# Optimization experiments

Measured on AMD Instinct MI355X. Metric: run time of the kernel, lower is better.

The kernel has to match this reference:

```python
import jax, jax.numpy as jnp
import numpy as np

N_HEAD = 16
THETA = 10000.0


def _freqs_cos_sin(head_dim, seq_len):
    # matches precompute_freqs_cis: freqs = 1/theta^(arange(0,dim,2)/dim), outer with t
    inv = 1.0 / (THETA ** (jnp.arange(0, head_dim, 2, dtype=jnp.float32) / head_dim))
    t = jnp.arange(seq_len, dtype=jnp.float32)
    ang = jnp.outer(t, inv)  # [L, head_dim//2]
    return jnp.cos(ang), jnp.sin(ang)


def _rope(x, cos, sin):
    # x: [B, H, L, D]; pairs are interleaved (view_as_complex on (..., D//2, 2))
    x1 = x[..., 0::2]
    x2 = x[..., 1::2]
    out_re = x1 * cos - x2 * sin
    out_im = x1 * sin + x2 * cos
    return jnp.stack([out_re, out_im], axis=-1).reshape(x.shape)


def setup_inputs() -> dict:
    key = jax.random.key(0)
    ks = jax.random.split(key, 11)
    B, L, D = 2, 2048, 1024
    s = 0.02
    return {
        "q": jax.random.normal(ks[0], (B, L, D), jnp.float32),
        "k": jax.random.normal(ks[1], (B, L, D), jnp.float32),
        "v": jax.random.normal(ks[2], (B, L, D), jnp.float32),
        "wq": jax.random.normal(ks[3], (D, D), jnp.float32) * s,
        "bq": jax.random.normal(ks[4], (D,), jnp.float32) * s,
        "wk": jax.random.normal(ks[5], (D, D), jnp.float32) * s,
        "bk": jax.random.normal(ks[6], (D,), jnp.float32) * s,
        "wv": jax.random.normal(ks[7], (D, D), jnp.float32) * s,
        "bv": jax.random.normal(ks[8], (D,), jnp.float32) * s,
        "wo": jax.random.normal(ks[9], (D, D), jnp.float32) * s,
        "bo": jax.random.normal(ks[10], (D,), jnp.float32) * s,
    }


def reference(q, k, v, wq, bq, wk, bk, wv, bv, wo, bo):
    B, L, D = q.shape
    Hd = D // N_HEAD
    # projections (nn.Linear: x @ W^T + b)
    qp = q @ wq.T + bq
    kp = k @ wk.T + bk
    vp = v @ wv.T + bv
    # split: [B, L, D] -> [B, H, L, Hd]
    def split(t):
        return t.reshape(B, L, N_HEAD, Hd).transpose(0, 2, 1, 3)
    qh, kh, vh = split(qp), split(kp), split(vp)
    cos, sin = _freqs_cos_sin(Hd, L)  # [L, Hd//2], broadcasts over B, H
    qh = _rope(qh, cos, sin)
    kh = _rope(kh, cos, sin)
    # scaled dot-product attention (no mask)
    scores = jnp.einsum("bhqd,bhkd->bhqk", qh, kh) / jnp.sqrt(jnp.float32(Hd))
    attn = jax.nn.softmax(scores, axis=-1)
    out = jnp.einsum("bhqk,bhkd->bhqd", attn, vh)
    # concat heads and output projection
    out = out.transpose(0, 2, 1, 3).reshape(B, L, D)
    return out @ wo.T + bo
```

## Files before the change

kernel.cpp:

```cpp
#include <hip/hip_runtime.h>
#include <hip/hip_bf16.h>
#include <math.h>

#define BB 2
#define LL 2048
#define DD 1024
#define NH 16
#define HD 64

typedef short v8s __attribute__((ext_vector_type(8)));
typedef float v4f __attribute__((ext_vector_type(4)));
typedef float v16f __attribute__((ext_vector_type(16)));

__device__ __forceinline__ float b2f(unsigned short b) {
  union { unsigned int u; float f; } c; c.u = ((unsigned int)b) << 16; return c.f;
}
__device__ __forceinline__ unsigned short f2b(float x) {
  union { float f; unsigned int u; } c; c.f = x;
  unsigned int u = c.u;
  u += 0x7fffu + ((u >> 16) & 1u);
  return (unsigned short)(u >> 16);
}
__device__ __forceinline__ unsigned int asu(float x) {
  union { float f; unsigned int u; } c; c.f = x; return c.u;
}
__device__ __forceinline__ unsigned int pk2(float lo, float hi) {
  return __builtin_amdgcn_perm(asu(hi), asu(lo), 0x07060302u);
}

__device__ __forceinline__ void gload16(const void* g, void* l) {
  __builtin_amdgcn_global_load_lds(
      (const __attribute__((address_space(1))) void*)g,
      (__attribute__((address_space(3))) void*)l, 16, 0, 0);
}

struct CastArgs { const float* s[7]; unsigned short* d[7]; };
__global__ void cast_all(CastArgs a) {
  int z = blockIdx.z;
  int t = (z < 12) ? (z >> 2) : (z - 9);
  int off = (z < 12) ? ((z & 3) << 18) : 0;
  int i = off + blockIdx.x * blockDim.x + threadIdx.x;
  float4 v = ((const float4*)a.s[t])[i];
  ushort4 o;
  o.x = f2b(v.x); o.y = f2b(v.y); o.z = f2b(v.z); o.w = f2b(v.w);
  ((ushort4*)a.d[t])[i] = o;
}

__global__ void freqs_kernel(float* __restrict__ ctab, float* __restrict__ stab) {
  int id = blockIdx.x * blockDim.x + threadIdx.x;
  int t = id >> 5, i = id & 31;
  float inv = powf(10000.0f, -(float)(2 * i) / 64.0f);
  float ang = (float)t * inv;
  ctab[id] = cosf(ang);
  stab[id] = sinf(ang);
}

template <typename OutT>
__device__ __forceinline__ void gemm_body(const unsigned short* __restrict__ X,
                                          const unsigned short* __restrict__ W,
                                          const float* __restrict__ bias,
                                          OutT* __restrict__ Y,
                                          int M, int N, int K) {
  __shared__ __align__(16) unsigned short As[128 * 64];
  __shared__ __align__(16) unsigned short Bs[128 * 64];
  const int tid = threadIdx.x;
  const int lane = tid & 63, wave = tid >> 6;
  const int quad = lane >> 4, l16 = lane & 15;
  const int bn0 = blockIdx.x * 128;
  const int bm0 = blockIdx.y * 128;
  const int wm = (wave >> 1) * 64, wn = (wave & 1) * 64;

  const v4f vzero = {0.f, 0.f, 0.f, 0.f};
  v4f acc[4][4];
#pragma unroll
  for (int i = 0; i < 4; ++i)
#pragma unroll
    for (int j = 0; j < 4; ++j) acc[i][j] = vzero;

  for (int k0 = 0; k0 < K; k0 += 64) {
#pragma unroll
    for (int c = 0; c < 4; ++c) {
      int id = c * 256 + tid;
      int r = id >> 3, cc = ((id & 7) ^ (r & 7)) * 8;
      gload16(X + (size_t)(bm0 + r) * K + k0 + cc, &As[id * 8]);
    }
#pragma unroll
    for (int c = 0; c < 4; ++c) {
      int id = c * 256 + tid;
      int r = id >> 3, cc = ((id & 7) ^ (r & 7)) * 8;
      gload16(W + (size_t)(bn0 + r) * K + k0 + cc, &Bs[id * 8]);
    }
    __syncthreads();
#pragma unroll
    for (int kh = 0; kh < 2; ++kh) {
      v8s a[4], b[4];
#pragma unroll
      for (int i = 0; i < 4; ++i) {
        int ra = wm + i * 16 + l16;
        int sa = (kh * 4 + quad) ^ (ra & 7);
        a[i] = *(const v8s*)&As[ra * 64 + sa * 8];
        int rb = wn + i * 16 + l16;
        int sb = (kh * 4 + quad) ^ (rb & 7);
        b[i] = *(const v8s*)&Bs[rb * 64 + sb * 8];
      }
#pragma unroll
      for (int mi = 0; mi < 4; ++mi)
#pragma unroll
        for (int ni = 0; ni < 4; ++ni)
          acc[mi][ni] = __builtin_amdgcn_mfma_f32_16x16x32_bf16(a[mi], b[ni], acc[mi][ni], 0, 0, 0);
    }
    __syncthreads();
  }

  float bv[4];
#pragma unroll
  for (int ni = 0; ni < 4; ++ni) bv[ni] = bias[bn0 + wn + ni * 16 + l16];
#pragma unroll
  for (int mi = 0; mi < 4; ++mi) {
#pragma unroll
    for (int r = 0; r < 4; ++r) {
      int row = bm0 + wm + mi * 16 + quad * 4 + r;
      size_t base = (size_t)row * N + bn0 + wn + l16;
#pragma unroll
      for (int ni = 0; ni < 4; ++ni) {
        float v = acc[mi][ni][r] + bv[ni];
        if constexpr (sizeof(OutT) == 2) {
          Y[base + ni * 16] = (OutT)f2b(v);
        } else {
          Y[base + ni * 16] = (OutT)v;
        }
      }
    }
  }
}

__global__ __launch_bounds__(256) void gemm_qkv(
    const unsigned short* x0, const unsigned short* w0, const float* b0, unsigned short* y0,
    const unsigned short* x1, const unsigned short* w1, const float* b1, unsigned short* y1,
    const unsigned short* x2, const unsigned short* w2, const float* b2, unsigned short* y2) {
  const unsigned short *X, *W; const float* Bp; unsigned short* Y;
  if (blockIdx.z == 0)      { X = x0; W = w0; Bp = b0; Y = y0; }
  else if (blockIdx.z == 1) { X = x1; W = w1; Bp = b1; Y = y1; }
  else                      { X = x2; W = w2; Bp = b2; Y = y2; }
  gemm_body<unsigned short>(X, W, Bp, Y, BB * LL, DD, DD);
}

__global__ __launch_bounds__(256) void gemm_out(
    const unsigned short* x, const unsigned short* w, const float* b, float* y) {
  gemm_body<float>(x, w, b, y, BB * LL, DD, DD);
}

__global__ void rope_kernel(const unsigned short* __restrict__ qp,
                            const unsigned short* __restrict__ kp,
                            unsigned short* __restrict__ qh,
                            unsigned short* __restrict__ kh,
                            const float* __restrict__ ctab,
                            const float* __restrict__ stab) {
  int id = blockIdx.x * blockDim.x + threadIdx.x;
  const unsigned short* src = (blockIdx.z == 0) ? qp : kp;
  unsigned short* dst = (blockIdx.z == 0) ? qh : kh;
  float sc = (blockIdx.z == 0) ? 0.125f : 1.0f;
  int i = id & 31;
  int l = (id >> 5) & (LL - 1);
  int h = (id >> 16) & (NH - 1);
  int b = id >> 20;
  ushort2 v = ((const ushort2*)(src + ((size_t)(b * LL + l) * DD + h * HD)))[i];
  float c = ctab[l * 32 + i], s = stab[l * 32 + i];
  float x1 = b2f(v.x), x2 = b2f(v.y);
  ushort2 o;
  o.x = f2b((x1 * c - x2 * s) * sc);
  o.y = f2b((x1 * s + x2 * c) * sc);
  ((ushort2*)(dst + (size_t)((b * NH + h) * LL + l) * HD))[i] = o;
}

__global__ void vtrans_kernel(const unsigned short* __restrict__ vp,
                              unsigned short* __restrict__ vt) {
  __shared__ unsigned short T[64][65];
  int bh = blockIdx.y;
  int b = bh >> 4, h = bh & 15;
  int l0 = blockIdx.x * 64;
  int t = threadIdx.x;
  int lr = t >> 2, seg = (t & 3) * 16;
  const unsigned short* src = vp + ((size_t)(b * LL + l0 + lr) * DD + h * HD + seg);
  ushort4 u0 = ((const ushort4*)src)[0];
  ushort4 u1 = ((const ushort4*)src)[1];
  ushort4 u2 = ((const ushort4*)src)[2];
  ushort4 u3 = ((const ushort4*)src)[3];
  T[lr][seg + 0] = u0.x;  T[lr][seg + 1] = u0.y;  T[lr][seg + 2] = u0.z;  T[lr][seg + 3] = u0.w;
  T[lr][seg + 4] = u1.x;  T[lr][seg + 5] = u1.y;  T[lr][seg + 6] = u1.z;  T[lr][seg + 7] = u1.w;
  T[lr][seg + 8] = u2.x;  T[lr][seg + 9] = u2.y;  T[lr][seg + 10] = u2.z; T[lr][seg + 11] = u2.w;
  T[lr][seg + 12] = u3.x; T[lr][seg + 13] = u3.y; T[lr][seg + 14] = u3.z; T[lr][seg + 15] = u3.w;
  __syncthreads();
  int dr = t >> 2, ls = (t & 3) * 16;
  unsigned short* dst = vt + ((size_t)(bh * HD + dr) * LL + l0 + ls);
  ushort4 o0, o1, o2, o3;
  o0.x = T[ls + 0][dr];  o0.y = T[ls + 1][dr];  o0.z = T[ls + 2][dr];  o0.w = T[ls + 3][dr];
  o1.x = T[ls + 4][dr];  o1.y = T[ls + 5][dr];  o1.z = T[ls + 6][dr];  o1.w = T[ls + 7][dr];
  o2.x = T[ls + 8][dr];  o2.y = T[ls + 9][dr];  o2.z = T[ls + 10][dr]; o2.w = T[ls + 11][dr];
  o3.x = T[ls + 12][dr]; o3.y = T[ls + 13][dr]; o3.z = T[ls + 14][dr]; o3.w = T[ls + 15][dr];
  ((ushort4*)dst)[0] = o0; ((ushort4*)dst)[2] = o1;
  ((ushort4*)dst)[1] = o2; ((ushort4*)dst)[3] = o3;
}

__global__ __launch_bounds__(256, 4) void flash_kernel(
    const unsigned short* __restrict__ qh,
    const unsigned short* __restrict__ kh,
    const unsigned short* __restrict__ vt,
    unsigned short* __restrict__ po, float* __restrict__ pl) {
  __shared__ __align__(16) unsigned short Ks[128 * 64];
  __shared__ __align__(16) unsigned short Vs[64 * 128];
  const int tid = threadIdx.x, wave = tid >> 6, lane = tid & 63;
  const int l32 = lane & 31, hf = lane >> 5;
  const int bh = blockIdx.y;
  const int split = blockIdx.z;
  const int q0 = blockIdx.x * 128;
  const unsigned short* qbase = qh + (size_t)bh * LL * HD;
  const unsigned short* kbase = kh + (size_t)bh * LL * HD;
  const unsigned short* vbase = vt + (size_t)bh * HD * LL;

  const int qrow = q0 + wave * 32 + l32;
  v8s qf[4];
#pragma unroll
  for (int ks2 = 0; ks2 < 4; ++ks2)
    qf[ks2] = *(const v8s*)(qbase + (size_t)qrow * HD + ks2 * 16 + hf * 8);

  v16f o0, o1;
#pragma unroll
  for (int i = 0; i < 16; ++i) { o0[i] = 0.0f; o1[i] = 0.0f; }
  float ls = 0.0f;

  const int kt0 = split * (LL / 2);
  for (int kt = kt0; kt < kt0 + LL / 2; kt += 128) {
#pragma unroll
    for (int i = 0; i < 4; ++i) {
      int id = i * 256 + tid;
      int r = id >> 3, c = (id & 7) ^ (r & 7);
      gload16(kbase + (size_t)(kt + r) * HD + c * 8, &Ks[id * 8]);
    }
#pragma unroll
    for (int i = 0; i < 4; ++i) {
      int id = i * 256 + tid;
      int r = id >> 4, c = (id & 15) ^ (r & 15);
      gload16(vbase + (size_t)r * LL + kt + c * 8, &Vs[id * 8]);
    }
    __syncthreads();

#pragma unroll
    for (int g = 0; g < 4; ++g) {
      v16f sc;
#pragma unroll
      for (int i = 0; i < 16; ++i) sc[i] = 0.0f;
#pragma unroll
      for (int ks2 = 0; ks2 < 4; ++ks2) {
        int row = g * 32 + l32;
        int slot = (ks2 * 2 + hf) ^ (lane & 7);
        v8s kf = *(const v8s*)&Ks[row * 64 + slot * 8];
        sc = __builtin_amdgcn_mfma_f32_32x32x16_bf16(kf, qf[ks2], sc, 0, 0, 0);
      }
      v16f e;
#pragma unroll
      for (int i = 0; i < 16; ++i) e[i] = __expf(sc[i]);
      float t0 = (e[0] + e[1]) + (e[2] + e[3]);
      float t1 = (e[4] + e[5]) + (e[6] + e[7]);
      float t2 = (e[8] + e[9]) + (e[10] + e[11]);
      float t3 = (e[12] + e[13]) + (e[14] + e[15]);
      ls += (t0 + t1) + (t2 + t3);
#pragma unroll
      for (int k2 = 0; k2 < 2; ++k2) {
        union { v8s v; unsigned int u[4]; } pb;
#pragma unroll
        for (int a = 0; a < 4; ++a)
          pb.u[a] = pk2(e[8 * k2 + 2 * a], e[8 * k2 + 2 * a + 1]);
        int k16 = g * 2 + k2;
        {
          int slotv = (k16 * 2 + hf) ^ (lane & 15);
          v8s vf = *(const v8s*)&Vs[l32 * 128 + slotv * 8];
          o0 = __builtin_amdgcn_mfma_f32_32x32x16_bf16(vf, pb.v, o0, 0, 0, 0);
        }
        {
          int slotv = (k16 * 2 + hf) ^ (lane & 15);
          v8s vf = *(const v8s*)&Vs[(32 + l32) * 128 + slotv * 8];
          o1 = __builtin_amdgcn_mfma_f32_32x32x16_bf16(vf, pb.v, o1, 0, 0, 0);
        }
      }
    }
    __syncthreads();
  }

  ls += __shfl_xor(ls, 32);
  if (hf == 0) pl[((size_t)split * 32 + bh) * LL + q0 + wave * 32 + l32] = ls;

  unsigned short* Wt = &Ks[wave * 2048];
#pragma unroll
  for (int dt = 0; dt < 2; ++dt)
#pragma unroll
    for (int r = 0; r < 16; ++r) {
      int dl = (r & 3) + 8 * (r >> 2) + 4 * hf;
      int d = dt * 32 + dl;
      int chunk = d >> 3, offw = d & 7;
      int slot = chunk ^ (l32 & 7);
      float val = (dt == 0) ? o0[r] : o1[r];
      Wt[l32 * 64 + slot * 8 + offw] = f2b(val);
    }
#pragma unroll
  for (int i = 0; i < 4; ++i) {
    int qr = lane >> 1;
    int chunk = (lane & 1) * 4 + i;
    int slot = chunk ^ (qr & 7);
    v8s dv = *(const v8s*)&Wt[qr * 64 + slot * 8];
    int token = q0 + wave * 32 + qr;
    *(v8s*)(po + (((size_t)split * 32 + bh) * LL + token) * HD + chunk * 8) = dv;
  }
}

__global__ void reduce_kernel(const unsigned short* __restrict__ po,
                              const float* __restrict__ pl,
                              unsigned short* __restrict__ attn) {
  int id = blockIdx.x * blockDim.x + threadIdx.x;
  int dg = id & 7, q = (id >> 3) & (LL - 1), bh = id >> 14;
  int b = bh >> 4, h = bh & 15;
  size_t base = ((size_t)bh * LL + q) * HD + dg * 8;
  v8s a = *(const v8s*)(po + base);
  v8s c = *(const v8s*)(po + base + (size_t)32 * LL * HD);
  float inv = 1.0f / (pl[bh * LL + q] + pl[(32 + bh) * LL + q]);
  v8s o;
#pragma unroll
  for (int j = 0; j < 8; ++j)
    o[j] = (short)f2b((b2f((unsigned short)a[j]) + b2f((unsigned short)c[j])) * inv);
  *(v8s*)(attn + ((size_t)(b * LL + q) * DD) + h * HD + dg * 8) = o;
}

extern "C" void kernel_launch(void* const* d_in, const int* in_sizes, int n_in,
                              void* d_out, int out_size, void* d_ws, size_t ws_size,
                              hipStream_t stream) {
  const float* q  = (const float*)d_in[0];
  const float* k  = (const float*)d_in[1];
  const float* v  = (const float*)d_in[2];
  const float* wq = (const float*)d_in[3];
  const float* bq = (const float*)d_in[4];
  const float* wk = (const float*)d_in[5];
  const float* bk = (const float*)d_in[6];
  const float* wv = (const float*)d_in[7];
  const float* bv = (const float*)d_in[8];
  const float* wo = (const float*)d_in[9];
  const float* bo = (const float*)d_in[10];
  float* out = (float*)d_out;

  size_t off = 0;
  char* wsb = (char*)d_ws;
  auto take = [&](size_t n) { void* p = wsb + off; off += n; return p; };
  const size_t SZT = (size_t)BB * LL * DD * 2;
  const size_t SZW = (size_t)DD * DD * 2;
  unsigned short* qb   = (unsigned short*)take(SZT);
  unsigned short* kb   = (unsigned short*)take(SZT);
  unsigned short* vb   = (unsigned short*)take(SZT);
  unsigned short* wqb  = (unsigned short*)take(SZW);
  unsigned short* wkb  = (unsigned short*)take(SZW);
  unsigned short* wvb  = (unsigned short*)take(SZW);
  unsigned short* wob  = (unsigned short*)take(SZW);
  unsigned short* qp   = (unsigned short*)take(SZT);
  unsigned short* kp   = (unsigned short*)take(SZT);
  unsigned short* vp   = (unsigned short*)take(SZT);
  unsigned short* qhh  = (unsigned short*)take(SZT);
  unsigned short* khh  = (unsigned short*)take(SZT);
  unsigned short* vtt  = (unsigned short*)take(SZT);
  unsigned short* attn = (unsigned short*)take(SZT);
  float* ctab = (float*)take((size_t)LL * 32 * 4);
  float* stab = (float*)take((size_t)LL * 32 * 4);
  unsigned short* po = (unsigned short*)wsb;
  float* pl = (float*)(wsb + ((size_t)16 << 20));

  CastArgs ca;
  ca.s[0] = q;  ca.s[1] = k;  ca.s[2] = v;  ca.s[3] = wq;
  ca.s[4] = wk; ca.s[5] = wv; ca.s[6] = wo;
  ca.d[0] = qb;  ca.d[1] = kb;  ca.d[2] = vb;  ca.d[3] = wqb;
  ca.d[4] = wkb; ca.d[5] = wvb; ca.d[6] = wob;
  cast_all<<<dim3(1024, 1, 16), 256, 0, stream>>>(ca);
  freqs_kernel<<<(LL * 32) / 256, 256, 0, stream>>>(ctab, stab);

  gemm_qkv<<<dim3(DD / 128, BB * LL / 128, 3), 256, 0, stream>>>(
      qb, wqb, bq, qp, kb, wkb, bk, kp, vb, wvb, bv, vp);

  rope_kernel<<<dim3((BB * NH * LL * 32) / 256, 1, 2), 256, 0, stream>>>(
      qp, kp, qhh, khh, ctab, stab);
  vtrans_kernel<<<dim3(LL / 64, BB * NH), 256, 0, stream>>>(vp, vtt);

  flash_kernel<<<dim3(LL / 128, BB * NH, 2), 256, 0, stream>>>(qhh, khh, vtt, po, pl);
  reduce_kernel<<<(32 * LL * 8) / 256, 256, 0, stream>>>(po, pl, attn);

  gemm_out<<<dim3(DD / 128, BB * LL / 128, 1), 256, 0, stream>>>(attn, wob, bo, out);
}
```

Before: 254.0 us.

## Process two query sub-tiles per wave in flash kernel and use exp2

```diff
diff --git a/kernel.cpp b/kernel.cpp
--- a/kernel.cpp
+++ b/kernel.cpp
@@ -27,6 +27,16 @@
 __device__ __forceinline__ unsigned int pk2(float lo, float hi) {
   return __builtin_amdgcn_perm(asu(hi), asu(lo), 0x07060302u);
 }
+
+#if defined(__has_builtin)
+#if __has_builtin(__builtin_amdgcn_exp2f)
+#define EXP2(x) __builtin_amdgcn_exp2f(x)
+#else
+#define EXP2(x) __expf((x) * 0.69314718056f)
+#endif
+#else
+#define EXP2(x) __expf((x) * 0.69314718056f)
+#endif
 
 __device__ __forceinline__ void gload16(const void* g, void* l) {
   __builtin_amdgcn_global_load_lds(
@@ -159,7 +169,7 @@
   int id = blockIdx.x * blockDim.x + threadIdx.x;
   const unsigned short* src = (blockIdx.z == 0) ? qp : kp;
   unsigned short* dst = (blockIdx.z == 0) ? qh : kh;
-  float sc = (blockIdx.z == 0) ? 0.125f : 1.0f;
+  float sc = (blockIdx.z == 0) ? 0.18033688f : 1.0f;
   int i = id & 31;
   int l = (id >> 5) & (LL - 1);
   int h = (id >> 16) & (NH - 1);
@@ -202,32 +212,39 @@
   ((ushort4*)dst)[1] = o2; ((ushort4*)dst)[3] = o3;
 }
 
-__global__ __launch_bounds__(256, 4) void flash_kernel(
+__global__ __launch_bounds__(256, 2) void flash_kernel(
     const unsigned short* __restrict__ qh,
     const unsigned short* __restrict__ kh,
     const unsigned short* __restrict__ vt,
     unsigned short* __restrict__ po, float* __restrict__ pl) {
-  __shared__ __align__(16) unsigned short Ks[128 * 64];
-  __shared__ __align__(16) unsigned short Vs[64 * 128];
+  __shared__ __align__(16) unsigned short S_[128 * 64 + 64 * 128];
+  unsigned short* Ks = S_;
+  unsigned short* Vs = S_ + 128 * 64;
   const int tid = threadIdx.x, wave = tid >> 6, lane = tid & 63;
   const int l32 = lane & 31, hf = lane >> 5;
   const int bh = blockIdx.y;
   const int split = blockIdx.z;
-  const int q0 = blockIdx.x * 128;
+  const int q0 = blockIdx.x * 256;
   const unsigned short* qbase = qh + (size_t)bh * LL * HD;
   const unsigned short* kbase = kh + (size_t)bh * LL * HD;
   const unsigned short* vbase = vt + (size_t)bh * HD * LL;
 
-  const int qrow = q0 + wave * 32 + l32;
-  v8s qf[4];
-#pragma unroll
-  for (int ks2 = 0; ks2 < 4; ++ks2)
-    qf[ks2] = *(const v8s*)(qbase + (size_t)qrow * HD + ks2 * 16 + hf * 8);
-
-  v16f o0, o1;
-#pragma unroll
-  for (int i = 0; i < 16; ++i) { o0[i] = 0.0f; o1[i] = 0.0f; }
-  float ls = 0.0f;
+  const int qrow = q0 + wave * 64 + l32;
+  v8s qf[2][4];
+#pragma unroll
+  for (int ks2 = 0; ks2 < 4; ++ks2) {
+    qf[0][ks2] = *(const v8s*)(qbase + (size_t)qrow * HD + ks2 * 16 + hf * 8);
+    qf[1][ks2] = *(const v8s*)(qbase + (size_t)(qrow + 32) * HD + ks2 * 16 + hf * 8);
+  }
+
+  v16f o[2][2];
+#pragma unroll
+  for (int qs = 0; qs < 2; ++qs)
+#pragma unroll
+    for (int dt = 0; dt < 2; ++dt)
+#pragma unroll
+      for (int i = 0; i < 16; ++i) o[qs][dt][i] = 0.0f;
+  float lsum[2] = {0.0f, 0.0f};
 
   const int kt0 = split * (LL / 2);
   for (int kt = kt0; kt < kt0 + LL / 2; kt += 128) {
@@ -247,70 +264,85 @@
 
 #pragma unroll
     for (int g = 0; g < 4; ++g) {
-      v16f sc;
-#pragma unroll
-      for (int i = 0; i < 16; ++i) sc[i] = 0.0f;
+      v16f sc0, sc1;
+#pragma unroll
+      for (int i = 0; i < 16; ++i) { sc0[i] = 0.0f; sc1[i] = 0.0f; }
 #pragma unroll
       for (int ks2 = 0; ks2 < 4; ++ks2) {
         int row = g * 32 + l32;
         int slot = (ks2 * 2 + hf) ^ (lane & 7);
         v8s kf = *(const v8s*)&Ks[row * 64 + slot * 8];
-        sc = __builtin_amdgcn_mfma_f32_32x32x16_bf16(kf, qf[ks2], sc, 0, 0, 0);
-      }
-      v16f e;
-#pragma unroll
-      for (int i = 0; i < 16; ++i) e[i] = __expf(sc[i]);
-      float t0 = (e[0] + e[1]) + (e[2] + e[3]);
-      float t1 = (e[4] + e[5]) + (e[6] + e[7]);
-      float t2 = (e[8] + e[9]) + (e[10] + e[11]);
-      float t3 = (e[12] + e[13]) + (e[14] + e[15]);
-      ls += (t0 + t1) + (t2 + t3);
+        sc0 = __builtin_amdgcn_mfma_f32_32x32x16_bf16(kf, qf[0][ks2], sc0, 0, 0, 0);
+        sc1 = __builtin_amdgcn_mfma_f32_32x32x16_bf16(kf, qf[1][ks2], sc1, 0, 0, 0);
+      }
+      v16f e0, e1;
+#pragma unroll
+      for (int i = 0; i < 16; ++i) { e0[i] = EXP2(sc0[i]); e1[i] = EXP2(sc1[i]); }
+      {
+        float a0 = (e0[0] + e0[1]) + (e0[2] + e0[3]);
+        float a1 = (e0[4] + e0[5]) + (e0[6] + e0[7]);
+        float a2 = (e0[8] + e0[9]) + (e0[10] + e0[11]);
+        float a3 = (e0[12] + e0[13]) + (e0[14] + e0[15]);
+        lsum[0] += (a0 + a1) + (a2 + a3);
+        float b0 = (e1[0] + e1[1]) + (e1[2] + e1[3]);
+        float b1 = (e1[4] + e1[5]) + (e1[6] + e1[7]);
+        float b2 = (e1[8] + e1[9]) + (e1[10] + e1[11]);
+        float b3 = (e1[12] + e1[13]) + (e1[14] + e1[15]);
+        lsum[1] += (b0 + b1) + (b2 + b3);
+      }
 #pragma unroll
       for (int k2 = 0; k2 < 2; ++k2) {
-        union { v8s v; unsigned int u[4]; } pb;
-#pragma unroll
-        for (int a = 0; a < 4; ++a)
-          pb.u[a] = pk2(e[8 * k2 + 2 * a], e[8 * k2 + 2 * a + 1]);
+        union { v8s v; unsigned int u[4]; } pb0, pb1;
+#pragma unroll
+        for (int a = 0; a < 4; ++a) {
+          pb0.u[a] = pk2(e0[8 * k2 + 2 * a], e0[8 * k2 + 2 * a + 1]);
+          pb1.u[a] = pk2(e1[8 * k2 + 2 * a], e1[8 * k2 + 2 * a + 1]);
+        }
         int k16 = g * 2 + k2;
-        {
-          int slotv = (k16 * 2 + hf) ^ (lane & 15);
-          v8s vf = *(const v8s*)&Vs[l32 * 128 + slotv * 8];
-          o0 = __builtin_amdgcn_mfma_f32_32x32x16_bf16(vf, pb.v, o0, 0, 0, 0);
-        }
-        {
-          int slotv = (k16 * 2 + hf) ^ (lane & 15);
-          v8s vf = *(const v8s*)&Vs[(32 + l32) * 128 + slotv * 8];
-          o1 = __builtin_amdgcn_mfma_f32_32x32x16_bf16(vf, pb.v, o1, 0, 0, 0);
-        }
+        int slotv = (k16 * 2 + hf) ^ (lane & 15);
+        v8s vf0 = *(const v8s*)&Vs[l32 * 128 + slotv * 8];
+        v8s vf1 = *(const v8s*)&Vs[(32 + l32) * 128 + slotv * 8];
+        o[0][0] = __builtin_amdgcn_mfma_f32_32x32x16_bf16(vf0, pb0.v, o[0][0], 0, 0, 0);
+        o[0][1] = __builtin_amdgcn_mfma_f32_32x32x16_bf16(vf1, pb0.v, o[0][1], 0, 0, 0);
+        o[1][0] = __builtin_amdgcn_mfma_f32_32x32x16_bf16(vf0, pb1.v, o[1][0], 0, 0, 0);
+        o[1][1] = __builtin_amdgcn_mfma_f32_32x32x16_bf16(vf1, pb1.v, o[1][1], 0, 0, 0);
       }
     }
     __syncthreads();
   }
 
-  ls += __shfl_xor(ls, 32);
-  if (hf == 0) pl[((size_t)split * 32 + bh) * LL + q0 + wave * 32 + l32] = ls;
-
-  unsigned short* Wt = &Ks[wave * 2048];
-#pragma unroll
-  for (int dt = 0; dt < 2; ++dt)
-#pragma unroll
-    for (int r = 0; r < 16; ++r) {
-      int dl = (r & 3) + 8 * (r >> 2) + 4 * hf;
-      int d = dt * 32 + dl;
-      int chunk = d >> 3, offw = d & 7;
-      int slot = chunk ^ (l32 & 7);
-      float val = (dt == 0) ? o0[r] : o1[r];
-      Wt[l32 * 64 + slot * 8 + offw] = f2b(val);
-    }
-#pragma unroll
-  for (int i = 0; i < 4; ++i) {
-    int qr = lane >> 1;
-    int chunk = (lane & 1) * 4 + i;
-    int slot = chunk ^ (qr & 7);
-    v8s dv = *(const v8s*)&Wt[qr * 64 + slot * 8];
-    int token = q0 + wave * 32 + qr;
-    *(v8s*)(po + (((size_t)split * 32 + bh) * LL + token) * HD + chunk * 8) = dv;
+  lsum[0] += __shfl_xor(lsum[0], 32);
+  lsum[1] += __shfl_xor(lsum[1], 32);
+  if (hf == 0) {
+    size_t lb = ((size_t)split * 32 + bh) * LL + q0 + wave * 64 + l32;
+    pl[lb] = lsum[0];
+    pl[lb + 32] = lsum[1];
   }
+
+  unsigned short* Wt = S_ + wave * 4096;
+#pragma unroll
+  for (int qs = 0; qs < 2; ++qs)
+#pragma unroll
+    for (int dt = 0; dt < 2; ++dt)
+#pragma unroll
+      for (int r = 0; r < 16; ++r) {
+        int dl = (r & 3) + 8 * (r >> 2) + 4 * hf;
+        int d = dt * 32 + dl;
+        int chunk = d >> 3, offw = d & 7;
+        int slot = chunk ^ (l32 & 7);
+        Wt[(qs * 32 + l32) * 64 + slot * 8 + offw] = f2b(o[qs][dt][r]);
+      }
+#pragma unroll
+  for (int qs = 0; qs < 2; ++qs)
+#pragma unroll
+    for (int i = 0; i < 4; ++i) {
+      int qr = qs * 32 + (lane >> 1);
+      int chunk = (lane & 1) * 4 + i;
+      int slot = chunk ^ ((lane >> 1) & 7);
+      v8s dv = *(const v8s*)&Wt[qr * 64 + slot * 8];
+      int token = q0 + wave * 64 + qr;
+      *(v8s*)(po + (((size_t)split * 32 + bh) * LL + token) * HD + chunk * 8) = dv;
+    }
 }
 
 __global__ void reduce_kernel(const unsigned short* __restrict__ po,
@@ -385,7 +417,7 @@
       qp, kp, qhh, khh, ctab, stab);
   vtrans_kernel<<<dim3(LL / 64, BB * NH), 256, 0, stream>>>(vp, vtt);
 
-  flash_kernel<<<dim3(LL / 128, BB * NH, 2), 256, 0, stream>>>(qhh, khh, vtt, po, pl);
+  flash_kernel<<<dim3(LL / 256, BB * NH, 2), 256, 0, stream>>>(qhh, khh, vtt, po, pl);
   reduce_kernel<<<(32 * LL * 8) / 256, 256, 0, stream>>>(po, pl, attn);
 
   gemm_out<<<dim3(DD / 128, BB * LL / 128, 1), 256, 0, stream>>>(attn, wob, bo, out);
```

Result: slower. 268.8 us (+5.8%).

## Drop flash split-K and reduce kernel, fuse prep kernels, use exp2

Applied to the files above, without the earlier changes.

```diff
diff --git a/kernel.cpp b/kernel.cpp
--- a/kernel.cpp
+++ b/kernel.cpp
@@ -28,15 +28,35 @@
   return __builtin_amdgcn_perm(asu(hi), asu(lo), 0x07060302u);
 }
 
+#if defined(__has_builtin)
+#if __has_builtin(__builtin_amdgcn_exp2f)
+#define EXP2(x) __builtin_amdgcn_exp2f(x)
+#else
+#define EXP2(x) __expf((x) * 0.69314718056f)
+#endif
+#else
+#define EXP2(x) __expf((x) * 0.69314718056f)
+#endif
+
 __device__ __forceinline__ void gload16(const void* g, void* l) {
   __builtin_amdgcn_global_load_lds(
       (const __attribute__((address_space(1))) void*)g,
       (__attribute__((address_space(3))) void*)l, 16, 0, 0);
 }
 
-struct CastArgs { const float* s[7]; unsigned short* d[7]; };
+struct CastArgs { const float* s[7]; unsigned short* d[7]; float* ct; float* st; };
 __global__ void cast_all(CastArgs a) {
   int z = blockIdx.z;
+  if (z == 16) {
+    if (blockIdx.x >= 256) return;
+    int id = blockIdx.x * blockDim.x + threadIdx.x;
+    int t = id >> 5, i = id & 31;
+    float inv = powf(10000.0f, -(float)(2 * i) / 64.0f);
+    float ang = (float)t * inv;
+    a.ct[id] = cosf(ang);
+    a.st[id] = sinf(ang);
+    return;
+  }
   int t = (z < 12) ? (z >> 2) : (z - 9);
   int off = (z < 12) ? ((z & 3) << 18) : 0;
   int i = off + blockIdx.x * blockDim.x + threadIdx.x;
@@ -44,15 +64,6 @@
   ushort4 o;
   o.x = f2b(v.x); o.y = f2b(v.y); o.z = f2b(v.z); o.w = f2b(v.w);
   ((ushort4*)a.d[t])[i] = o;
-}
-
-__global__ void freqs_kernel(float* __restrict__ ctab, float* __restrict__ stab) {
-  int id = blockIdx.x * blockDim.x + threadIdx.x;
-  int t = id >> 5, i = id & 31;
-  float inv = powf(10000.0f, -(float)(2 * i) / 64.0f);
-  float ang = (float)t * inv;
-  ctab[id] = cosf(ang);
-  stab[id] = sinf(ang);
 }
 
 template <typename OutT>
@@ -150,35 +161,37 @@
   gemm_body<float>(x, w, b, y, BB * LL, DD, DD);
 }
 
-__global__ void rope_kernel(const unsigned short* __restrict__ qp,
+__global__ void prep_kernel(const unsigned short* __restrict__ qp,
                             const unsigned short* __restrict__ kp,
+                            const unsigned short* __restrict__ vp,
                             unsigned short* __restrict__ qh,
                             unsigned short* __restrict__ kh,
+                            unsigned short* __restrict__ vt,
                             const float* __restrict__ ctab,
                             const float* __restrict__ stab) {
-  int id = blockIdx.x * blockDim.x + threadIdx.x;
-  const unsigned short* src = (blockIdx.z == 0) ? qp : kp;
-  unsigned short* dst = (blockIdx.z == 0) ? qh : kh;
-  float sc = (blockIdx.z == 0) ? 0.125f : 1.0f;
-  int i = id & 31;
-  int l = (id >> 5) & (LL - 1);
-  int h = (id >> 16) & (NH - 1);
-  int b = id >> 20;
-  ushort2 v = ((const ushort2*)(src + ((size_t)(b * LL + l) * DD + h * HD)))[i];
-  float c = ctab[l * 32 + i], s = stab[l * 32 + i];
-  float x1 = b2f(v.x), x2 = b2f(v.y);
-  ushort2 o;
-  o.x = f2b((x1 * c - x2 * s) * sc);
-  o.y = f2b((x1 * s + x2 * c) * sc);
-  ((ushort2*)(dst + (size_t)((b * NH + h) * LL + l) * HD))[i] = o;
-}
-
-__global__ void vtrans_kernel(const unsigned short* __restrict__ vp,
-                              unsigned short* __restrict__ vt) {
+  if (blockIdx.z < 2) {
+    int id = blockIdx.x * blockDim.x + threadIdx.x;
+    const unsigned short* src = (blockIdx.z == 0) ? qp : kp;
+    unsigned short* dst = (blockIdx.z == 0) ? qh : kh;
+    float sc = (blockIdx.z == 0) ? 0.18033688f : 1.0f;
+    int i = id & 31;
+    int l = (id >> 5) & (LL - 1);
+    int h = (id >> 16) & (NH - 1);
+    int b = id >> 20;
+    ushort2 v = ((const ushort2*)(src + ((size_t)(b * LL + l) * DD + h * HD)))[i];
+    float c = ctab[l * 32 + i], s = stab[l * 32 + i];
+    float x1 = b2f(v.x), x2 = b2f(v.y);
+    ushort2 o;
+    o.x = f2b((x1 * c - x2 * s) * sc);
+    o.y = f2b((x1 * s + x2 * c) * sc);
+    ((ushort2*)(dst + (size_t)((b * NH + h) * LL + l) * HD))[i] = o;
+    return;
+  }
+  if (blockIdx.x >= 1024) return;
   __shared__ unsigned short T[64][65];
-  int bh = blockIdx.y;
+  int bh = blockIdx.x >> 5;
   int b = bh >> 4, h = bh & 15;
-  int l0 = blockIdx.x * 64;
+  int l0 = (blockIdx.x & 31) * 64;
   int t = threadIdx.x;
   int lr = t >> 2, seg = (t & 3) * 16;
   const unsigned short* src = vp + ((size_t)(b * LL + l0 + lr) * DD + h * HD + seg);
@@ -206,13 +219,13 @@
     const unsigned short* __restrict__ qh,
     const unsigned short* __restrict__ kh,
     const unsigned short* __restrict__ vt,
-    unsigned short* __restrict__ po, float* __restrict__ pl) {
-  __shared__ __align__(16) unsigned short Ks[128 * 64];
-  __shared__ __align__(16) unsigned short Vs[64 * 128];
+    unsigned short* __restrict__ attn) {
+  __shared__ __align__(16) unsigned short S_[128 * 64 + 64 * 128];
+  unsigned short* Ks = S_;
+  unsigned short* Vs = S_ + 128 * 64;
   const int tid = threadIdx.x, wave = tid >> 6, lane = tid & 63;
   const int l32 = lane & 31, hf = lane >> 5;
-  const int bh = blockIdx.y;
-  const int split = blockIdx.z;
+  const int bh = blockIdx.y, b = bh >> 4, hd = bh & 15;
   const int q0 = blockIdx.x * 128;
   const unsigned short* qbase = qh + (size_t)bh * LL * HD;
   const unsigned short* kbase = kh + (size_t)bh * LL * HD;
@@ -229,8 +242,7 @@
   for (int i = 0; i < 16; ++i) { o0[i] = 0.0f; o1[i] = 0.0f; }
   float ls = 0.0f;
 
-  const int kt0 = split * (LL / 2);
-  for (int kt = kt0; kt < kt0 + LL / 2; kt += 128) {
+  for (int kt = 0; kt < LL; kt += 128) {
 #pragma unroll
     for (int i = 0; i < 4; ++i) {
       int id = i * 256 + tid;
@@ -259,7 +271,7 @@
       }
       v16f e;
 #pragma unroll
-      for (int i = 0; i < 16; ++i) e[i] = __expf(sc[i]);
+      for (int i = 0; i < 16; ++i) e[i] = EXP2(sc[i]);
       float t0 = (e[0] + e[1]) + (e[2] + e[3]);
       float t1 = (e[4] + e[5]) + (e[6] + e[7]);
       float t2 = (e[8] + e[9]) + (e[10] + e[11]);
@@ -272,23 +284,18 @@
         for (int a = 0; a < 4; ++a)
           pb.u[a] = pk2(e[8 * k2 + 2 * a], e[8 * k2 + 2 * a + 1]);
         int k16 = g * 2 + k2;
-        {
-          int slotv = (k16 * 2 + hf) ^ (lane & 15);
-          v8s vf = *(const v8s*)&Vs[l32 * 128 + slotv * 8];
-          o0 = __builtin_amdgcn_mfma_f32_32x32x16_bf16(vf, pb.v, o0, 0, 0, 0);
-        }
-        {
-          int slotv = (k16 * 2 + hf) ^ (lane & 15);
-          v8s vf = *(const v8s*)&Vs[(32 + l32) * 128 + slotv * 8];
-          o1 = __builtin_amdgcn_mfma_f32_32x32x16_bf16(vf, pb.v, o1, 0, 0, 0);
-        }
+        int slotv = (k16 * 2 + hf) ^ (lane & 15);
+        v8s vf0 = *(const v8s*)&Vs[l32 * 128 + slotv * 8];
+        v8s vf1 = *(const v8s*)&Vs[(32 + l32) * 128 + slotv * 8];
+        o0 = __builtin_amdgcn_mfma_f32_32x32x16_bf16(vf0, pb.v, o0, 0, 0, 0);
+        o1 = __builtin_amdgcn_mfma_f32_32x32x16_bf16(vf1, pb.v, o1, 0, 0, 0);
       }
     }
     __syncthreads();
   }
 
   ls += __shfl_xor(ls, 32);
-  if (hf == 0) pl[((size_t)split * 32 + bh) * LL + q0 + wave * 32 + l32] = ls;
+  float inv = 1.0f / ls;
 
   unsigned short* Wt = &Ks[wave * 2048];
 #pragma unroll
@@ -300,7 +307,7 @@
       int chunk = d >> 3, offw = d & 7;
       int slot = chunk ^ (l32 & 7);
       float val = (dt == 0) ? o0[r] : o1[r];
-      Wt[l32 * 64 + slot * 8 + offw] = f2b(val);
+      Wt[l32 * 64 + slot * 8 + offw] = f2b(val * inv);
     }
 #pragma unroll
   for (int i = 0; i < 4; ++i) {
@@ -309,25 +316,8 @@
     int slot = chunk ^ (qr & 7);
     v8s dv = *(const v8s*)&Wt[qr * 64 + slot * 8];
     int token = q0 + wave * 32 + qr;
-    *(v8s*)(po + (((size_t)split * 32 + bh) * LL + token) * HD + chunk * 8) = dv;
-  }
-}
-
-__global__ void reduce_kernel(const unsigned short* __restrict__ po,
-                              const float* __restrict__ pl,
-                              unsigned short* __restrict__ attn) {
-  int id = blockIdx.x * blockDim.x + threadIdx.x;
-  int dg = id & 7, q = (id >> 3) & (LL - 1), bh = id >> 14;
-  int b = bh >> 4, h = bh & 15;
-  size_t base = ((size_t)bh * LL + q) * HD + dg * 8;
-  v8s a = *(const v8s*)(po + base);
-  v8s c = *(const v8s*)(po + base + (size_t)32 * LL * HD);
-  float inv = 1.0f / (pl[bh * LL + q] + pl[(32 + bh) * LL + q]);
-  v8s o;
-#pragma unroll
-  for (int j = 0; j < 8; ++j)
-    o[j] = (short)f2b((b2f((unsigned short)a[j]) + b2f((unsigned short)c[j])) * inv);
-  *(v8s*)(attn + ((size_t)(b * LL + q) * DD) + h * HD + dg * 8) = o;
+    *(v8s*)(attn + ((size_t)(b * LL + token) * DD) + hd * HD + chunk * 8) = dv;
+  }
 }
 
 extern "C" void kernel_launch(void* const* d_in, const int* in_sizes, int n_in,
@@ -367,26 +357,22 @@
   unsigned short* attn = (unsigned short*)take(SZT);
   float* ctab = (float*)take((size_t)LL * 32 * 4);
   float* stab = (float*)take((size_t)LL * 32 * 4);
-  unsigned short* po = (unsigned short*)wsb;
-  float* pl = (float*)(wsb + ((size_t)16 << 20));
 
   CastArgs ca;
   ca.s[0] = q;  ca.s[1] = k;  ca.s[2] = v;  ca.s[3] = wq;
   ca.s[4] = wk; ca.s[5] = wv; ca.s[6] = wo;
   ca.d[0] = qb;  ca.d[1] = kb;  ca.d[2] = vb;  ca.d[3] = wqb;
   ca.d[4] = wkb; ca.d[5] = wvb; ca.d[6] = wob;
-  cast_all<<<dim3(1024, 1, 16), 256, 0, stream>>>(ca);
-  freqs_kernel<<<(LL * 32) / 256, 256, 0, stream>>>(ctab, stab);
+  ca.ct = ctab; ca.st = stab;
+  cast_all<<<dim3(1024, 1, 17), 256, 0, stream>>>(ca);
 
   gemm_qkv<<<dim3(DD / 128, BB * LL / 128, 3), 256, 0, stream>>>(
       qb, wqb, bq, qp, kb, wkb, bk, kp, vb, wvb, bv, vp);
 
-  rope_kernel<<<dim3((BB * NH * LL * 32) / 256, 1, 2), 256, 0, stream>>>(
-      qp, kp, qhh, khh, ctab, stab);
-  vtrans_kernel<<<dim3(LL / 64, BB * NH), 256, 0, stream>>>(vp, vtt);
-
-  flash_kernel<<<dim3(LL / 128, BB * NH, 2), 256, 0, stream>>>(qhh, khh, vtt, po, pl);
-  reduce_kernel<<<(32 * LL * 8) / 256, 256, 0, stream>>>(po, pl, attn);
+  prep_kernel<<<dim3((BB * NH * LL * 32) / 256, 1, 3), 256, 0, stream>>>(
+      qp, kp, vp, qhh, khh, vtt, ctab, stab);
+
+  flash_kernel<<<dim3(LL / 128, BB * NH), 256, 0, stream>>>(qhh, khh, vtt, attn);
 
   gemm_out<<<dim3(DD / 128, BB * LL / 128, 1), 256, 0, stream>>>(attn, wob, bo, out);
 }
```

New measurement: 243.1 us. 1.04x faster.
